# Kernel optimization log

Hardware: AMD Instinct MI355X
Metric: run time of the kernel (lower is better)

## Reference

```python
import jax, jax.numpy as jnp
import numpy as np

INPUT_SIZE = 128
OUTPUT_SIZE = 128
HIDDEN = 8
BATCH = 1024
N = INPUT_SIZE * OUTPUT_SIZE  # number of tiny subnetworks


def setup_inputs() -> dict:
    key = jax.random.key(0)
    ks = jax.random.split(key, 7)
    s = 0.5  # modest init scale
    return {
        "x": jax.random.normal(ks[0], (BATCH, INPUT_SIZE), dtype=jnp.float32),
        "W1": jax.random.normal(ks[1], (N, HIDDEN, 1), dtype=jnp.float32) * s,
        "b1": jax.random.normal(ks[2], (N, HIDDEN), dtype=jnp.float32) * s,
        "W2": jax.random.normal(ks[3], (N, HIDDEN, HIDDEN), dtype=jnp.float32) * s,
        "b2": jax.random.normal(ks[4], (N, HIDDEN), dtype=jnp.float32) * s,
        "W3": jax.random.normal(ks[5], (N, 1, HIDDEN), dtype=jnp.float32) * s,
        "b3": jax.random.normal(ks[6], (N, 1), dtype=jnp.float32) * s,
    }


def reference(x, W1, b1, W2, b2, W3, b3):
    # x: [B, input_size]. Subnet n = i*output_size + o consumes feature i.
    B = x.shape[0]
    # x.T repeat_interleave(output_size, dim=0).unsqueeze(-1) -> [N, B, 1]
    xe = jnp.repeat(x.T, OUTPUT_SIZE, axis=0)[:, :, None]
    # torch Linear: y = x @ W.T + b, batched over subnet dim n
    h = jax.nn.relu(jnp.einsum('nbi,nhi->nbh', xe, W1) + b1[:, None, :])
    h = jax.nn.relu(jnp.einsum('nbi,nhi->nbh', h, W2) + b2[:, None, :])
    o = jnp.einsum('nbh,noh->nbo', h, W3) + b3[:, None, :]  # [N, B, 1]
    o = o[..., 0].reshape(INPUT_SIZE, OUTPUT_SIZE, B)
    return o.sum(axis=0).T  # [B, output_size]
```

## Files before the change

### kernel.cpp

```cpp
#include <hip/hip_runtime.h>

#define INPUT_SIZE 128
#define OUTPUT_SIZE 128
#define HIDDEN 8
#define BATCH 1024

#define ICH 32
#define IPC (INPUT_SIZE / ICH)
#define TPB 128
#define BPT 8
#define SLOT 60

typedef __fp16 half2v __attribute__((ext_vector_type(2)));
typedef unsigned int u4v __attribute__((ext_vector_type(4)));

#if defined(__has_builtin)
#if __has_builtin(__builtin_amdgcn_fdot2)
#define HAS_FDOT2 1
#endif
#endif
#ifndef HAS_FDOT2
#define HAS_FDOT2 0
#endif

static __device__ __forceinline__ half2v bch2(unsigned int u) {
    return __builtin_bit_cast(half2v, u);
}
static __device__ __forceinline__ unsigned int pk(float a, float b) {
    return __builtin_bit_cast(unsigned int, __builtin_amdgcn_cvt_pkrtz(a, b));
}

__global__ void transpose_x_kernel(const float* __restrict__ x,
                                   float* __restrict__ xT) {
    __shared__ float tile[32][33];
    const int i0 = blockIdx.x * 32;
    const int b0 = blockIdx.y * 32;
    const int tx = threadIdx.x;
    const int ty = threadIdx.y;
#pragma unroll
    for (int r = ty; r < 32; r += 8)
        tile[r][tx] = x[(b0 + r) * INPUT_SIZE + (i0 + tx)];
    __syncthreads();
#pragma unroll
    for (int r = ty; r < 32; r += 8)
        xT[(i0 + r) * BATCH + (b0 + tx)] = tile[tx][r];
}

template <bool PARTIALS>
__global__ __launch_bounds__(TPB, 3)
void mlpkan_kernel(const float* __restrict__ xT,
                   const float* __restrict__ W1, const float* __restrict__ b1,
                   const float* __restrict__ W2, const float* __restrict__ b2,
                   const float* __restrict__ W3, const float* __restrict__ b3,
                   float* __restrict__ partials, float* __restrict__ out) {
    __shared__ __attribute__((aligned(16))) float wlds[IPC * SLOT];

    const int o   = blockIdx.x;
    const int ic  = blockIdx.y;
    const int tid = threadIdx.x;

    {
        const int ii  = tid >> 4;
        const int idx = tid & 15;
        if (ii < IPC) {
            const int n = (ic * IPC + ii) * OUTPUT_SIZE + o;
            float* d = &wlds[ii * SLOT];
            if (idx == 0) {
                const float4 a = *(const float4*)(W1 + (size_t)n * 8);
                const float4 c = *(const float4*)(W1 + (size_t)n * 8 + 4);
                u4v p = {pk(a.x, a.y), pk(a.z, a.w), pk(c.x, c.y), pk(c.z, c.w)};
                *(u4v*)(d + 0) = p;
            } else if (idx == 1) {
                const float4 a = *(const float4*)(b1 + (size_t)n * 8);
                const float4 c = *(const float4*)(b1 + (size_t)n * 8 + 4);
                u4v p = {pk(a.x, a.y), pk(a.z, a.w), pk(c.x, c.y), pk(c.z, c.w)};
                *(u4v*)(d + 4) = p;
            } else if (idx == 2) {
                *(float4*)(d + 8)  = *(const float4*)(b2 + (size_t)n * 8);
            } else if (idx == 3) {
                *(float4*)(d + 12) = *(const float4*)(b2 + (size_t)n * 8 + 4);
            } else if (idx == 4) {
                *(float4*)(d + 16) = *(const float4*)(W3 + (size_t)n * 8);
            } else if (idx == 5) {
                *(float4*)(d + 20) = *(const float4*)(W3 + (size_t)n * 8 + 4);
            } else if (idx == 6) {
                d[24] = b3[n];
            } else if (idx >= 8) {
                const int h = idx - 8;
                const float4 a = *(const float4*)(W2 + (size_t)n * 64 + h * 8);
                const float4 c = *(const float4*)(W2 + (size_t)n * 64 + h * 8 + 4);
                u4v p = {pk(a.x, a.y), pk(a.z, a.w), pk(c.x, c.y), pk(c.z, c.w)};
                *(u4v*)(d + 28 + 4 * h) = p;
            }
        }
    }
    __syncthreads();

    float acc[BPT];
#pragma unroll
    for (int j = 0; j < BPT; ++j) acc[j] = 0.0f;

    const unsigned base_off = (unsigned)(size_t)(&wlds[0]);

#pragma unroll 1
    for (int ii = 0; ii < IPC; ++ii) {
        const int i = ic * IPC + ii;

        const float4 sA = *(const float4*)(xT + (size_t)i * BATCH + 4 * tid);
        const float4 sB = *(const float4*)(xT + (size_t)i * BATCH + 512 + 4 * tid);
        const float sjs[BPT] = {sA.x, sA.y, sA.z, sA.w, sB.x, sB.y, sB.z, sB.w};

        u4v w1q, b1q, w2q0, w2q1, w2q2, w2q3, w2q4, w2q5, w2q6, w2q7;
        float4 b2qa, b2qb, w3qa, w3qb;
        float b3r;
        const unsigned lds_off = base_off + (unsigned)(ii * (SLOT * 4));
        asm volatile(
            "ds_read_b128 %0, %15 offset:0\n\t"
            "ds_read_b128 %1, %15 offset:16\n\t"
            "ds_read_b128 %2, %15 offset:32\n\t"
            "ds_read_b128 %3, %15 offset:48\n\t"
            "ds_read_b128 %4, %15 offset:64\n\t"
            "ds_read_b128 %5, %15 offset:80\n\t"
            "ds_read_b32  %6, %15 offset:96\n\t"
            "ds_read_b128 %7, %15 offset:112\n\t"
            "ds_read_b128 %8, %15 offset:128\n\t"
            "ds_read_b128 %9, %15 offset:144\n\t"
            "ds_read_b128 %10, %15 offset:160\n\t"
            "ds_read_b128 %11, %15 offset:176\n\t"
            "ds_read_b128 %12, %15 offset:192\n\t"
            "ds_read_b128 %13, %15 offset:208\n\t"
            "ds_read_b128 %14, %15 offset:224\n\t"
            "s_waitcnt lgkmcnt(0)"
            : "=&v"(w1q), "=&v"(b1q), "=&v"(b2qa), "=&v"(b2qb),
              "=&v"(w3qa), "=&v"(w3qb), "=&v"(b3r),
              "=&v"(w2q0), "=&v"(w2q1), "=&v"(w2q2), "=&v"(w2q3),
              "=&v"(w2q4), "=&v"(w2q5), "=&v"(w2q6), "=&v"(w2q7)
            : "v"(lds_off)
            : "memory");

        const half2v zero2 = {(__fp16)0.0f, (__fp16)0.0f};

        half2v h1p[BPT][4];
#pragma unroll
        for (int j = 0; j < BPT; ++j) {
            const half2v xx = __builtin_amdgcn_cvt_pkrtz(sjs[j], sjs[j]);
#pragma unroll
            for (int q = 0; q < 4; ++q) {
                const half2v v = bch2(w1q[q]) * xx + bch2(b1q[q]);
                h1p[j][q] = __builtin_elementwise_max(v, zero2);
            }
        }

        float v3[BPT];
#pragma unroll
        for (int j = 0; j < BPT; ++j) v3[j] = 0.0f;

#if HAS_FDOT2
#define ROWDOT(t, RQ, j) \
        t = __builtin_amdgcn_fdot2(bch2(RQ[0]), h1p[j][0], t, false); \
        t = __builtin_amdgcn_fdot2(bch2(RQ[1]), h1p[j][1], t, false); \
        t = __builtin_amdgcn_fdot2(bch2(RQ[2]), h1p[j][2], t, false); \
        t = __builtin_amdgcn_fdot2(bch2(RQ[3]), h1p[j][3], t, false);
#else
#define ROWDOT(t, RQ, j) { \
        const half2v r0_ = bch2(RQ[0]), r1_ = bch2(RQ[1]); \
        const half2v r2_ = bch2(RQ[2]), r3_ = bch2(RQ[3]); \
        t = fmaf((float)r0_[0], (float)h1p[j][0][0], t); \
        t = fmaf((float)r0_[1], (float)h1p[j][0][1], t); \
        t = fmaf((float)r1_[0], (float)h1p[j][1][0], t); \
        t = fmaf((float)r1_[1], (float)h1p[j][1][1], t); \
        t = fmaf((float)r2_[0], (float)h1p[j][2][0], t); \
        t = fmaf((float)r2_[1], (float)h1p[j][2][1], t); \
        t = fmaf((float)r3_[0], (float)h1p[j][3][0], t); \
        t = fmaf((float)r3_[1], (float)h1p[j][3][1], t); }
#endif

#define L23(h, RQ) { \
        const float b2h_ = (h < 4) ? b2qa[h] : b2qb[(h) - 4]; \
        const float w3h_ = (h < 4) ? w3qa[h] : w3qb[(h) - 4]; \
        _Pragma("unroll") \
        for (int j = 0; j < BPT; ++j) { \
            float t = b2h_; \
            ROWDOT(t, RQ, j); \
            v3[j] = fmaf(w3h_, fmaxf(t, 0.0f), v3[j]); \
        } }

        L23(0, w2q0) L23(1, w2q1) L23(2, w2q2) L23(3, w2q3)
        L23(4, w2q4) L23(5, w2q5) L23(6, w2q6) L23(7, w2q7)
#undef L23
#undef ROWDOT

#pragma unroll
        for (int j = 0; j < BPT; ++j)
            acc[j] += v3[j] + b3r;
    }

    if (PARTIALS) {
        float* base = partials + ((size_t)ic * OUTPUT_SIZE + o) * BATCH;
        float4 pa = {acc[0], acc[1], acc[2], acc[3]};
        float4 pb = {acc[4], acc[5], acc[6], acc[7]};
        *(float4*)(base + 4 * tid)       = pa;
        *(float4*)(base + 512 + 4 * tid) = pb;
    } else {
#pragma unroll
        for (int j = 0; j < BPT; ++j) {
            const int b = (j < 4) ? (4 * tid + j) : (512 + 4 * tid + (j - 4));
            atomicAdd(&out[(size_t)b * OUTPUT_SIZE + o], acc[j]);
        }
    }
}

__global__ void reduce_kernel(const float* __restrict__ partials,
                              float* __restrict__ out) {
    __shared__ float tile[32][33];
    const int o0 = blockIdx.x * 32;
    const int b0 = blockIdx.y * 32;
    const int tx = threadIdx.x;
    const int ty = threadIdx.y;
#pragma unroll
    for (int r = ty; r < 32; r += 16) {
        float v = 0.0f;
#pragma unroll
        for (int icc = 0; icc < ICH; ++icc)
            v += partials[((size_t)icc * OUTPUT_SIZE + o0 + r) * BATCH + b0 + tx];
        tile[r][tx] = v;
    }
    __syncthreads();
#pragma unroll
    for (int r = ty; r < 32; r += 16)
        out[(size_t)(b0 + r) * OUTPUT_SIZE + o0 + tx] = tile[tx][r];
}

__global__ __launch_bounds__(256, 2)
void mlpkan_naive(const float* __restrict__ x,
                  const float* __restrict__ W1, const float* __restrict__ b1,
                  const float* __restrict__ W2, const float* __restrict__ b2,
                  const float* __restrict__ W3, const float* __restrict__ b3,
                  float* __restrict__ out) {
    const int o = blockIdx.x;
    const int b = blockIdx.y * 256 + threadIdx.x;
    float acc = 0.0f;
    for (int i = 0; i < INPUT_SIZE; ++i) {
        const int n = i * OUTPUT_SIZE + o;
        const float s = x[b * INPUT_SIZE + i];
        float h1[8], h2[8];
#pragma unroll
        for (int k = 0; k < 8; ++k)
            h1[k] = fmaxf(fmaf(W1[(size_t)n * 8 + k], s, b1[(size_t)n * 8 + k]), 0.0f);
#pragma unroll
        for (int h = 0; h < 8; ++h) {
            float v = b2[(size_t)n * 8 + h];
#pragma unroll
            for (int k = 0; k < 8; ++k)
                v = fmaf(W2[(size_t)n * 64 + h * 8 + k], h1[k], v);
            h2[h] = fmaxf(v, 0.0f);
        }
        float v = b3[n];
#pragma unroll
        for (int k = 0; k < 8; ++k)
            v = fmaf(W3[(size_t)n * 8 + k], h2[k], v);
        acc += v;
    }
    out[(size_t)b * OUTPUT_SIZE + o] = acc;
}

extern "C" void kernel_launch(void* const* d_in, const int* in_sizes, int n_in,
                              void* d_out, int out_size, void* d_ws, size_t ws_size,
                              hipStream_t stream) {
    const float* x  = (const float*)d_in[0];
    const float* W1 = (const float*)d_in[1];
    const float* b1 = (const float*)d_in[2];
    const float* W2 = (const float*)d_in[3];
    const float* b2 = (const float*)d_in[4];
    const float* W3 = (const float*)d_in[5];
    const float* b3 = (const float*)d_in[6];
    float* out = (float*)d_out;

    const size_t xt_elems   = (size_t)INPUT_SIZE * BATCH;
    const size_t part_elems = (size_t)ICH * OUTPUT_SIZE * BATCH;
    const size_t need_bytes = (xt_elems + part_elems) * sizeof(float);

    if (ws_size >= need_bytes) {
        float* xT       = (float*)d_ws;
        float* partials = xT + xt_elems;

        transpose_x_kernel<<<dim3(4, 32), dim3(32, 8), 0, stream>>>(x, xT);
        mlpkan_kernel<true><<<dim3(OUTPUT_SIZE, ICH), TPB, 0, stream>>>(
            xT, W1, b1, W2, b2, W3, b3, partials, out);
        reduce_kernel<<<dim3(4, 32), dim3(32, 16), 0, stream>>>(partials, out);
    } else {
        mlpkan_naive<<<dim3(OUTPUT_SIZE, BATCH / 256), 256, 0, stream>>>(
            x, W1, b1, W2, b2, W3, b3, out);
    }
}
```

Before: 109.6 us.

## Restructure MLP-KAN kernel: fewer input chunks, more threads, interleaved LDS weight layout

Cuts input chunks from 32 to 8, so each block handles 16 subnets, and raises threads per block to 256 with 4 batch elements each. The LDS slot layout is repacked so each W2 row sits next to its b2 and W3 scalars. The inline-asm bulk LDS read is replaced by per-row compiler-generated loads inside a loop over the hidden units. This shrinks the partial-sum buffer and reduce work and lowers register pressure for higher occupancy, but leaves less ILP per thread and fewer blocks.

```diff
diff --git a/kernel.cpp b/kernel.cpp
--- a/kernel.cpp
+++ b/kernel.cpp
@@ -5,11 +5,11 @@
 #define HIDDEN 8
 #define BATCH 1024
 
-#define ICH 32
+#define ICH 8
 #define IPC (INPUT_SIZE / ICH)
-#define TPB 128
-#define BPT 8
-#define SLOT 60
+#define TPB 256
+#define BPT 4
+#define SLOT 76
 
 typedef __fp16 half2v __attribute__((ext_vector_type(2)));
 typedef unsigned int u4v __attribute__((ext_vector_type(4)));
@@ -47,7 +47,7 @@
 }
 
 template <bool PARTIALS>
-__global__ __launch_bounds__(TPB, 3)
+__global__ __launch_bounds__(TPB, 4)
 void mlpkan_kernel(const float* __restrict__ xT,
                    const float* __restrict__ W1, const float* __restrict__ b1,
                    const float* __restrict__ W2, const float* __restrict__ b2,
@@ -62,36 +62,28 @@
     {
         const int ii  = tid >> 4;
         const int idx = tid & 15;
-        if (ii < IPC) {
-            const int n = (ic * IPC + ii) * OUTPUT_SIZE + o;
-            float* d = &wlds[ii * SLOT];
-            if (idx == 0) {
-                const float4 a = *(const float4*)(W1 + (size_t)n * 8);
-                const float4 c = *(const float4*)(W1 + (size_t)n * 8 + 4);
-                u4v p = {pk(a.x, a.y), pk(a.z, a.w), pk(c.x, c.y), pk(c.z, c.w)};
-                *(u4v*)(d + 0) = p;
-            } else if (idx == 1) {
-                const float4 a = *(const float4*)(b1 + (size_t)n * 8);
-                const float4 c = *(const float4*)(b1 + (size_t)n * 8 + 4);
-                u4v p = {pk(a.x, a.y), pk(a.z, a.w), pk(c.x, c.y), pk(c.z, c.w)};
-                *(u4v*)(d + 4) = p;
-            } else if (idx == 2) {
-                *(float4*)(d + 8)  = *(const float4*)(b2 + (size_t)n * 8);
-            } else if (idx == 3) {
-                *(float4*)(d + 12) = *(const float4*)(b2 + (size_t)n * 8 + 4);
-            } else if (idx == 4) {
-                *(float4*)(d + 16) = *(const float4*)(W3 + (size_t)n * 8);
-            } else if (idx == 5) {
-                *(float4*)(d + 20) = *(const float4*)(W3 + (size_t)n * 8 + 4);
-            } else if (idx == 6) {
-                d[24] = b3[n];
-            } else if (idx >= 8) {
-                const int h = idx - 8;
-                const float4 a = *(const float4*)(W2 + (size_t)n * 64 + h * 8);
-                const float4 c = *(const float4*)(W2 + (size_t)n * 64 + h * 8 + 4);
-                u4v p = {pk(a.x, a.y), pk(a.z, a.w), pk(c.x, c.y), pk(c.z, c.w)};
-                *(u4v*)(d + 28 + 4 * h) = p;
-            }
+        const int n   = (ic * IPC + ii) * OUTPUT_SIZE + o;
+        float* d = &wlds[ii * SLOT];
+        if (idx == 0) {
+            const float4 a = *(const float4*)(W1 + (size_t)n * 8);
+            const float4 c = *(const float4*)(W1 + (size_t)n * 8 + 4);
+            u4v p = {pk(a.x, a.y), pk(a.z, a.w), pk(c.x, c.y), pk(c.z, c.w)};
+            *(u4v*)(d + 0) = p;
+        } else if (idx == 1) {
+            const float4 a = *(const float4*)(b1 + (size_t)n * 8);
+            const float4 c = *(const float4*)(b1 + (size_t)n * 8 + 4);
+            u4v p = {pk(a.x, a.y), pk(a.z, a.w), pk(c.x, c.y), pk(c.z, c.w)};
+            *(u4v*)(d + 4) = p;
+        } else if (idx == 2) {
+            d[8] = b3[n];
+        } else if (idx >= 8) {
+            const int h = idx - 8;
+            const float4 a = *(const float4*)(W2 + (size_t)n * 64 + h * 8);
+            const float4 c = *(const float4*)(W2 + (size_t)n * 64 + h * 8 + 4);
+            u4v p = {pk(a.x, a.y), pk(a.z, a.w), pk(c.x, c.y), pk(c.z, c.w)};
+            *(u4v*)(d + 12 + 8 * h) = p;
+            d[12 + 8 * h + 4] = b2[(size_t)n * 8 + h];
+            d[12 + 8 * h + 5] = W3[(size_t)n * 8 + h];
         }
     }
     __syncthreads();
@@ -99,45 +91,17 @@
     float acc[BPT];
 #pragma unroll
     for (int j = 0; j < BPT; ++j) acc[j] = 0.0f;
-
-    const unsigned base_off = (unsigned)(size_t)(&wlds[0]);
 
 #pragma unroll 1
     for (int ii = 0; ii < IPC; ++ii) {
         const int i = ic * IPC + ii;
-
-        const float4 sA = *(const float4*)(xT + (size_t)i * BATCH + 4 * tid);
-        const float4 sB = *(const float4*)(xT + (size_t)i * BATCH + 512 + 4 * tid);
-        const float sjs[BPT] = {sA.x, sA.y, sA.z, sA.w, sB.x, sB.y, sB.z, sB.w};
-
-        u4v w1q, b1q, w2q0, w2q1, w2q2, w2q3, w2q4, w2q5, w2q6, w2q7;
-        float4 b2qa, b2qb, w3qa, w3qb;
-        float b3r;
-        const unsigned lds_off = base_off + (unsigned)(ii * (SLOT * 4));
-        asm volatile(
-            "ds_read_b128 %0, %15 offset:0\n\t"
-            "ds_read_b128 %1, %15 offset:16\n\t"
-            "ds_read_b128 %2, %15 offset:32\n\t"
-            "ds_read_b128 %3, %15 offset:48\n\t"
-            "ds_read_b128 %4, %15 offset:64\n\t"
-            "ds_read_b128 %5, %15 offset:80\n\t"
-            "ds_read_b32  %6, %15 offset:96\n\t"
-            "ds_read_b128 %7, %15 offset:112\n\t"
-            "ds_read_b128 %8, %15 offset:128\n\t"
-            "ds_read_b128 %9, %15 offset:144\n\t"
-            "ds_read_b128 %10, %15 offset:160\n\t"
-            "ds_read_b128 %11, %15 offset:176\n\t"
-            "ds_read_b128 %12, %15 offset:192\n\t"
-            "ds_read_b128 %13, %15 offset:208\n\t"
-            "ds_read_b128 %14, %15 offset:224\n\t"
-            "s_waitcnt lgkmcnt(0)"
-            : "=&v"(w1q), "=&v"(b1q), "=&v"(b2qa), "=&v"(b2qb),
-              "=&v"(w3qa), "=&v"(w3qb), "=&v"(b3r),
-              "=&v"(w2q0), "=&v"(w2q1), "=&v"(w2q2), "=&v"(w2q3),
-              "=&v"(w2q4), "=&v"(w2q5), "=&v"(w2q6), "=&v"(w2q7)
-            : "v"(lds_off)
-            : "memory");
-
+        const float* w = &wlds[ii * SLOT];
+
+        const float4 sv = *(const float4*)(xT + (size_t)i * BATCH + 4 * tid);
+        const float sjs[BPT] = {sv.x, sv.y, sv.z, sv.w};
+
+        const u4v w1q = *(const u4v*)(w + 0);
+        const u4v b1q = *(const u4v*)(w + 4);
         const half2v zero2 = {(__fp16)0.0f, (__fp16)0.0f};
 
         half2v h1p[BPT][4];
@@ -155,41 +119,40 @@
 #pragma unroll
         for (int j = 0; j < BPT; ++j) v3[j] = 0.0f;
 
+#pragma unroll
+        for (int h = 0; h < HIDDEN; ++h) {
+            const u4v    row = *(const u4v*)(w + 12 + 8 * h);
+            const float2 bw  = *(const float2*)(w + 12 + 8 * h + 4);
+            const float b2h = bw.x;
+            const float w3h = bw.y;
+#pragma unroll
+            for (int j = 0; j < BPT; ++j) {
 #if HAS_FDOT2
-#define ROWDOT(t, RQ, j) \
-        t = __builtin_amdgcn_fdot2(bch2(RQ[0]), h1p[j][0], t, false); \
-        t = __builtin_amdgcn_fdot2(bch2(RQ[1]), h1p[j][1], t, false); \
-        t = __builtin_amdgcn_fdot2(bch2(RQ[2]), h1p[j][2], t, false); \
-        t = __builtin_amdgcn_fdot2(bch2(RQ[3]), h1p[j][3], t, false);
+                float t = b2h;
+                t = __builtin_amdgcn_fdot2(bch2(row[0]), h1p[j][0], t, false);
+                t = __builtin_amdgcn_fdot2(bch2(row[1]), h1p[j][1], t, false);
+                t = __builtin_amdgcn_fdot2(bch2(row[2]), h1p[j][2], t, false);
+                t = __builtin_amdgcn_fdot2(bch2(row[3]), h1p[j][3], t, false);
 #else
-#define ROWDOT(t, RQ, j) { \
-        const half2v r0_ = bch2(RQ[0]), r1_ = bch2(RQ[1]); \
-        const half2v r2_ = bch2(RQ[2]), r3_ = bch2(RQ[3]); \
-        t = fmaf((float)r0_[0], (float)h1p[j][0][0], t); \
-        t = fmaf((float)r0_[1], (float)h1p[j][0][1], t); \
-        t = fmaf((float)r1_[0], (float)h1p[j][1][0], t); \
-        t = fmaf((float)r1_[1], (float)h1p[j][1][1], t); \
-        t = fmaf((float)r2_[0], (float)h1p[j][2][0], t); \
-        t = fmaf((float)r2_[1], (float)h1p[j][2][1], t); \
-        t = fmaf((float)r3_[0], (float)h1p[j][3][0], t); \
-        t = fmaf((float)r3_[1], (float)h1p[j][3][1], t); }
-#endif
-
-#define L23(h, RQ) { \
-        const float b2h_ = (h < 4) ? b2qa[h] : b2qb[(h) - 4]; \
-        const float w3h_ = (h < 4) ? w3qa[h] : w3qb[(h) - 4]; \
-        _Pragma("unroll") \
-        for (int j = 0; j < BPT; ++j) { \
-            float t = b2h_; \
-            ROWDOT(t, RQ, j); \
-            v3[j] = fmaf(w3h_, fmaxf(t, 0.0f), v3[j]); \
-        } }
-
-        L23(0, w2q0) L23(1, w2q1) L23(2, w2q2) L23(3, w2q3)
-        L23(4, w2q4) L23(5, w2q5) L23(6, w2q6) L23(7, w2q7)
-#undef L23
-#undef ROWDOT
-
+                float t = b2h;
+                {
+                    const half2v r0 = bch2(row[0]), r1 = bch2(row[1]);
+                    const half2v r2 = bch2(row[2]), r3 = bch2(row[3]);
+                    t = fmaf((float)r0[0], (float)h1p[j][0][0], t);
+                    t = fmaf((float)r0[1], (float)h1p[j][0][1], t);
+                    t = fmaf((float)r1[0], (float)h1p[j][1][0], t);
+                    t = fmaf((float)r1[1], (float)h1p[j][1][1], t);
+                    t = fmaf((float)r2[0], (float)h1p[j][2][0], t);
+                    t = fmaf((float)r2[1], (float)h1p[j][2][1], t);
+                    t = fmaf((float)r3[0], (float)h1p[j][3][0], t);
+                    t = fmaf((float)r3[1], (float)h1p[j][3][1], t);
+                }
+#endif
+                v3[j] = fmaf(w3h, fmaxf(t, 0.0f), v3[j]);
+            }
+        }
+
+        const float b3r = w[8];
 #pragma unroll
         for (int j = 0; j < BPT; ++j)
             acc[j] += v3[j] + b3r;
@@ -198,15 +161,11 @@
     if (PARTIALS) {
         float* base = partials + ((size_t)ic * OUTPUT_SIZE + o) * BATCH;
         float4 pa = {acc[0], acc[1], acc[2], acc[3]};
-        float4 pb = {acc[4], acc[5], acc[6], acc[7]};
-        *(float4*)(base + 4 * tid)       = pa;
-        *(float4*)(base + 512 + 4 * tid) = pb;
+        *(float4*)(base + 4 * tid) = pa;
     } else {
 #pragma unroll
-        for (int j = 0; j < BPT; ++j) {
-            const int b = (j < 4) ? (4 * tid + j) : (512 + 4 * tid + (j - 4));
-            atomicAdd(&out[(size_t)b * OUTPUT_SIZE + o], acc[j]);
-        }
+        for (int j = 0; j < BPT; ++j)
+            atomicAdd(&out[(size_t)(4 * tid + j) * OUTPUT_SIZE + o], acc[j]);
     }
 }
 
```

Result: no change. 107.4 us (-1.9%).
